# Optimization experiments

Measured on AMD Instinct MI355X. Metric: run time of the kernel, lower is better.

The kernel has to match this reference:

```python
import jax, jax.numpy as jnp
import numpy as np

B, S, D = 2, 2048, 2048
H, G = 32, 8            # n_heads, n_kv_groups
HD = D // H             # head_dim = 64
GS = H // G             # group_size = 4


def _rope(t, cos, sin):
    # t: (B, h, S, HD); cos/sin: (S, HD), start_pos = 0
    half = t.shape[-1] // 2
    rot = jnp.concatenate([-t[..., half:], t[..., :half]], axis=-1)
    return t * cos[None, None] + rot * sin[None, None]


def setup_inputs() -> dict:
    key = jax.random.key(0)
    ks = jax.random.split(key, 7)
    x = jax.random.normal(ks[0], (B, S, D), jnp.float32)
    cos = jax.random.normal(ks[1], (S, HD), jnp.float32)
    sin = jax.random.normal(ks[2], (S, HD), jnp.float32)
    mask = jnp.zeros((S, S), jnp.bool_)
    Wq = jax.random.normal(ks[3], (D, D), jnp.float32) * 0.02
    Wk = jax.random.normal(ks[4], (G * HD, D), jnp.float32) * 0.02
    Wv = jax.random.normal(ks[5], (G * HD, D), jnp.float32) * 0.02
    Wo = jax.random.normal(ks[6], (D, D), jnp.float32) * 0.02
    return {"x": x, "cos": cos, "sin": sin, "mask": mask,
            "Wq": Wq, "Wk": Wk, "Wv": Wv, "Wo": Wo}


def reference(x, cos, sin, mask, Wq, Wk, Wv, Wo):
    b, s, d = x.shape
    # projections (nn.Linear: y = x @ W.T)
    q = (x @ Wq.T).reshape(b, s, H, HD).transpose(0, 2, 1, 3)   # (b,H,s,HD)
    k = (x @ Wk.T).reshape(b, s, G, HD).transpose(0, 2, 1, 3)   # (b,G,s,HD)
    v = (x @ Wv.T).reshape(b, s, G, HD).transpose(0, 2, 1, 3)   # (b,G,s,HD)
    q = _rope(q, cos, sin)
    k = _rope(k, cos, sin)
    # GQA: heads grouped contiguously per kv group (equivalent to repeat_interleave on kv)
    qg = q.reshape(b, G, GS, s, HD)
    scores = jnp.einsum('bgmsd,bgtd->bgmst', qg, k) / jnp.sqrt(jnp.float32(HD))
    # NOTE: original calls non-inplace masked_fill and DISCARDS the result,
    # so the mask has no effect on the output; reproduced faithfully.
    attn = jax.nn.softmax(scores, axis=-1)
    y = jnp.einsum('bgmst,bgtd->bgmsd', attn, v)
    y = y.reshape(b, H, s, HD).transpose(0, 2, 1, 3).reshape(b, s, d)
    return y @ Wo.T
```

## Files before the change

kernel.cpp:

```cpp
#include <hip/hip_runtime.h>
#include <hip/hip_bf16.h>
#include <stdint.h>

#define B_ 2
#define S_ 2048
#define D_ 2048
#define H_ 32
#define G_ 8
#define HD_ 64
#define KVD (G_*HD_)

typedef unsigned short u16;
typedef unsigned int u32;
typedef __attribute__((ext_vector_type(8))) short s8v;
typedef __attribute__((ext_vector_type(4))) float f4v;

static __device__ __forceinline__ float bf2f(u16 u){ return __uint_as_float(((u32)u)<<16); }
static __device__ __forceinline__ u16 f2bf(float f){
  u32 b = __float_as_uint(f);
  return (u16)((b + 0x7FFFu + ((b>>16)&1u)) >> 16);
}
static __device__ __forceinline__ u32 pk2bf(float a, float b){
  float2 f2 = make_float2(a, b);
  __hip_bfloat162 h = __float22bfloat162_rn(f2);
  return *(u32*)&h;
}

struct CvtArgs {
  const float *x, *wq, *wk, *wv, *wo;
  u16 *xb, *wqb, *wkb, *wvb, *wob;
};
__global__ void k_cvt5(CvtArgs a){
  const int E0 = 2097152;
  const int E1 = E0 + 1048576;
  const int E2 = E1 + 262144;
  const int E3 = E2 + 262144;
  const int E4 = E3 + 1048576;
  int u = blockIdx.x*blockDim.x + threadIdx.x;
  int stride = gridDim.x*blockDim.x;
  for (; u < E4; u += stride){
    const float* s; u16* d; int off;
    if      (u < E0){ s = a.x;  d = a.xb;  off = u; }
    else if (u < E1){ s = a.wq; d = a.wqb; off = u - E0; }
    else if (u < E2){ s = a.wk; d = a.wkb; off = u - E1; }
    else if (u < E3){ s = a.wv; d = a.wvb; off = u - E2; }
    else            { s = a.wo; d = a.wob; off = u - E3; }
    float4 f = *(const float4*)(s + (long)off*4);
    uint2 o;
    o.x = (u32)f2bf(f.x) | ((u32)f2bf(f.y)<<16);
    o.y = (u32)f2bf(f.z) | ((u32)f2bf(f.w)<<16);
    *(uint2*)(d + (long)off*4) = o;
  }
}

template<int MODE>
__global__ __launch_bounds__(256) void k_gemm(const u16* __restrict__ A,
    const u16* __restrict__ Bw, const u16* __restrict__ Bw2,
    void* __restrict__ C, void* __restrict__ C2,
    const float* __restrict__ cs, const float* __restrict__ sn,
    int M, int N, int K){
  bool second = (MODE == 2) && (blockIdx.z == 1);
  if (second) Bw = Bw2;
  __shared__ u16 As[128*32];
  __shared__ u16 Bs[128*32];
  const int tid = threadIdx.x;
  const int lane = tid & 63, wid = tid >> 6;
  const int l15 = lane & 15, l4 = lane >> 4;
  const int wr = wid >> 1, wc = wid & 1;
  const long Arow0 = (long)blockIdx.x * 128;
  const long Brow0 = (long)blockIdx.y * 128;
  f4v acc[4][4] = {};
  for (int k0 = 0; k0 < K; k0 += 32){
    if (k0) __syncthreads();
    #pragma unroll
    for (int is = 0; is < 2; ++is){
      int c = (is*4 + wid)*64 + lane;
      int row = c >> 2, slot = c & 3;
      int ko = slot ^ (row & 3);
      const u16* srcA = A + (Arow0 + row)*K + k0 + ko*8;
      const u16* srcB = Bw + (Brow0 + row)*K + k0 + ko*8;
      __builtin_amdgcn_global_load_lds((__attribute__((address_space(1))) void*)(void*)srcA,
          (__attribute__((address_space(3))) void*)(As + (is*4 + wid)*512), 16, 0, 0);
      __builtin_amdgcn_global_load_lds((__attribute__((address_space(1))) void*)(void*)srcB,
          (__attribute__((address_space(3))) void*)(Bs + (is*4 + wid)*512), 16, 0, 0);
    }
    __syncthreads();
    s8v af[4], bf[4];
    #pragma unroll
    for (int m = 0; m < 4; ++m){
      int row = wr*64 + m*16 + l15;
      af[m] = *(const s8v*)((const char*)As + row*64 + ((l4 ^ (row & 3))<<4));
    }
    #pragma unroll
    for (int n = 0; n < 4; ++n){
      int col = wc*64 + n*16 + l15;
      bf[n] = *(const s8v*)((const char*)Bs + col*64 + ((l4 ^ (col & 3))<<4));
    }
    #pragma unroll
    for (int m = 0; m < 4; ++m)
      #pragma unroll
      for (int n = 0; n < 4; ++n)
        acc[m][n] = __builtin_amdgcn_mfma_f32_16x16x32_bf16(af[m], bf[n], acc[m][n], 0, 0, 0);
  }

  if (MODE == 0){
    #pragma unroll
    for (int m = 0; m < 4; ++m)
      #pragma unroll
      for (int n = 0; n < 4; ++n)
        #pragma unroll
        for (int i = 0; i < 4; ++i){
          long r = Arow0 + wr*64 + m*16 + l4*4 + i;
          long c = Brow0 + wc*64 + n*16 + l15;
          ((float*)C)[r*N + c] = acc[m][n][i];
        }
  } else if (MODE == 1 || !second){
    u16* out = (u16*)C;
    #pragma unroll
    for (int m = 0; m < 4; ++m){
      long r0 = Arow0 + wr*64 + m*16 + l4*4;
      #pragma unroll
      for (int i = 0; i < 4; ++i){
        int s = (int)((r0 + i) & (S_-1));
        const float* cb = cs + s*64 + l15;
        const float* sb = sn + s*64 + l15;
        #pragma unroll
        for (int n = 0; n < 2; ++n){
          float c0 = cb[n*16],      s0v = sb[n*16];
          float c1 = cb[n*16 + 32], s1v = sb[n*16 + 32];
          float t0 = acc[m][n][i], t1 = acc[m][n+2][i];
          long cA = Brow0 + wc*64 + n*16 + l15;
          out[(r0+i)*N + cA]      = f2bf(t0*c0 - t1*s0v);
          out[(r0+i)*N + cA + 32] = f2bf(t1*c1 + t0*s1v);
        }
      }
    }
  } else {
    u16* vt = (u16*)C2;
    int g = (int)((Brow0 + wc*64) >> 6);
    #pragma unroll
    for (int m = 0; m < 4; ++m){
      long r0 = Arow0 + wr*64 + m*16 + l4*4;
      int b = (int)(r0 >> 11), s0 = (int)(r0 & (S_-1));
      #pragma unroll
      for (int n = 0; n < 4; ++n){
        int d = n*16 + l15;
        uint2 w;
        w.x = (u32)f2bf(acc[m][n][0]) | ((u32)f2bf(acc[m][n][1])<<16);
        w.y = (u32)f2bf(acc[m][n][2]) | ((u32)f2bf(acc[m][n][3])<<16);
        *(uint2*)(vt + ((long)(b*G_ + g)*64 + d)*S_ + s0) = w;
      }
    }
  }
}

__global__ __launch_bounds__(512) void k_fattn(const u16* __restrict__ q,
    const u16* __restrict__ k, const u16* __restrict__ vt, u16* __restrict__ o){
  __shared__ u16 Ks[3][64*64];
  __shared__ u16 VTs[3][64*64];
  __shared__ u16 Ps[8][32*64];
  const int tid = threadIdx.x, lane = tid & 63, wid = tid >> 6;
  const int l15 = lane & 15, l4 = lane >> 4;
  const int qt = blockIdx.x, h = blockIdx.y, b = blockIdx.z;
  const int g = h >> 2;
  const long qrow0 = (long)b*S_ + qt*256 + wid*32;
  const float C1 = 0.125f * 1.44269504f;
  const float C0 = -8.0f * 1.44269504f;
  const int NT = S_/64;

  s8v aq[2][2];
  #pragma unroll
  for (int mf = 0; mf < 2; ++mf)
    #pragma unroll
    for (int kf = 0; kf < 2; ++kf)
      aq[mf][kf] = *(const s8v*)(q + (qrow0 + mf*16 + l15)*D_ + h*64 + kf*32 + l4*8);

  const int c = wid*64 + lane;
  const int srow = c >> 3, ko = (c & 7) ^ (srow & 7);
  const u16* ksrc0 = k  + ((long)b*S_ + srow)*KVD + g*64 + ko*8;
  const u16* vsrc0 = vt + ((long)(b*G_ + g)*64 + srow)*S_ + ko*8;

  auto stage = [&](int kt, int slot){
    __builtin_amdgcn_global_load_lds(
        (__attribute__((address_space(1))) void*)(void*)(ksrc0 + (long)kt*64*KVD),
        (__attribute__((address_space(3))) void*)(&Ks[slot][wid*512]), 16, 0, 0);
    __builtin_amdgcn_global_load_lds(
        (__attribute__((address_space(1))) void*)(void*)(vsrc0 + kt*64),
        (__attribute__((address_space(3))) void*)(&VTs[slot][wid*512]), 16, 0, 0);
  };

  f4v oacc[2][4] = {};
  float lsum[2] = {0.f, 0.f};

  stage(0, 0);
  stage(1, 1);
  int cur = 0, nxt = 2;
  for (int kt = 0; kt < NT; ++kt){
    asm volatile("s_waitcnt vmcnt(2)" ::: "memory");
    __builtin_amdgcn_s_barrier();
    __builtin_amdgcn_sched_barrier(0);
    stage((kt + 2) & (NT - 1), nxt);
    const u16* KsB = Ks[cur];
    const u16* VsB = VTs[cur];

    s8v bk[4][2];
    #pragma unroll
    for (int nf = 0; nf < 4; ++nf){
      int key = nf*16 + l15;
      #pragma unroll
      for (int kf = 0; kf < 2; ++kf)
        bk[nf][kf] = *(const s8v*)((const char*)KsB + key*128 + (((kf*4 + l4) ^ (key & 7))<<4));
    }
    f4v sacc[2][4] = {};
    __builtin_amdgcn_s_setprio(1);
    #pragma unroll
    for (int mf = 0; mf < 2; ++mf)
      #pragma unroll
      for (int nf = 0; nf < 4; ++nf)
        #pragma unroll
        for (int kf = 0; kf < 2; ++kf)
          sacc[mf][nf] = __builtin_amdgcn_mfma_f32_16x16x32_bf16(bk[nf][kf], aq[mf][kf], sacc[mf][nf], 0, 0, 0);
    __builtin_amdgcn_s_setprio(0);

    #pragma unroll
    for (int mf = 0; mf < 2; ++mf){
      int r = mf*16 + l15;
      char* pbase = (char*)Ps[wid] + r*128 + (l4 & 1)*8;
      float rs = 0.f;
      #pragma unroll
      for (int nf = 0; nf < 4; ++nf){
        float p0 = __builtin_amdgcn_exp2f(fmaf(sacc[mf][nf][0], C1, C0));
        float p1 = __builtin_amdgcn_exp2f(fmaf(sacc[mf][nf][1], C1, C0));
        float p2 = __builtin_amdgcn_exp2f(fmaf(sacc[mf][nf][2], C1, C0));
        float p3 = __builtin_amdgcn_exp2f(fmaf(sacc[mf][nf][3], C1, C0));
        rs += (p0 + p1) + (p2 + p3);
        uint2 w; w.x = pk2bf(p0, p1); w.y = pk2bf(p2, p3);
        int slot = nf*2 + (l4 >> 1);
        *(uint2*)(pbase + ((slot ^ (r & 7))<<4)) = w;
      }
      lsum[mf] += rs;
    }

    s8v ap[2][2];
    #pragma unroll
    for (int mf = 0; mf < 2; ++mf){
      int r = mf*16 + l15;
      #pragma unroll
      for (int kf = 0; kf < 2; ++kf)
        ap[mf][kf] = *(const s8v*)((const char*)Ps[wid] + r*128 + (((kf*4 + l4) ^ (r & 7))<<4));
    }
    __builtin_amdgcn_s_setprio(1);
    #pragma unroll
    for (int nd = 0; nd < 4; ++nd){
      int d = nd*16 + l15;
      #pragma unroll
      for (int kf = 0; kf < 2; ++kf){
        s8v bv = *(const s8v*)((const char*)VsB + d*128 + (((kf*4 + l4) ^ (d & 7))<<4));
        #pragma unroll
        for (int mf = 0; mf < 2; ++mf)
          oacc[mf][nd] = __builtin_amdgcn_mfma_f32_16x16x32_bf16(ap[mf][kf], bv, oacc[mf][nd], 0, 0, 0);
      }
    }
    __builtin_amdgcn_s_setprio(0);
    cur = (cur == 2) ? 0 : cur + 1;
    nxt = (nxt == 2) ? 0 : nxt + 1;
  }

  #pragma unroll
  for (int mf = 0; mf < 2; ++mf){
    lsum[mf] += __shfl_xor(lsum[mf], 16);
    lsum[mf] += __shfl_xor(lsum[mf], 32);
  }
  #pragma unroll
  for (int mf = 0; mf < 2; ++mf){
    float li0 = 1.f / __shfl(lsum[mf], l4*4 + 0);
    float li1 = 1.f / __shfl(lsum[mf], l4*4 + 1);
    float li2 = 1.f / __shfl(lsum[mf], l4*4 + 2);
    float li3 = 1.f / __shfl(lsum[mf], l4*4 + 3);
    #pragma unroll
    for (int nd = 0; nd < 4; ++nd){
      long r = qrow0 + mf*16 + l4*4;
      int cc = h*64 + nd*16 + l15;
      o[(r+0)*D_ + cc] = f2bf(oacc[mf][nd][0]*li0);
      o[(r+1)*D_ + cc] = f2bf(oacc[mf][nd][1]*li1);
      o[(r+2)*D_ + cc] = f2bf(oacc[mf][nd][2]*li2);
      o[(r+3)*D_ + cc] = f2bf(oacc[mf][nd][3]*li3);
    }
  }
}

extern "C" void kernel_launch(void* const* d_in, const int* in_sizes, int n_in,
                              void* d_out, int out_size, void* d_ws, size_t ws_size,
                              hipStream_t stream){
  const float* x    = (const float*)d_in[0];
  const float* cosp = (const float*)d_in[1];
  const float* sinp = (const float*)d_in[2];
  const float* Wq = (const float*)d_in[4];
  const float* Wk = (const float*)d_in[5];
  const float* Wv = (const float*)d_in[6];
  const float* Wo = (const float*)d_in[7];

  char* ws = (char*)d_ws;
  size_t off = 0;
  auto alloc = [&](size_t bytes)->char*{
    char* p = ws + off; off += (bytes + 255) & ~(size_t)255; return p;
  };
  u16* xb  = (u16*)alloc((size_t)8388608*2);
  u16* wqb = (u16*)alloc((size_t)4194304*2);
  u16* wkb = (u16*)alloc((size_t)1048576*2);
  u16* wvb = (u16*)alloc((size_t)1048576*2);
  u16* wob = (u16*)alloc((size_t)4194304*2);
  u16* qb  = (u16*)alloc((size_t)8388608*2);
  u16* kb  = (u16*)alloc((size_t)2097152*2);
  u16* vtb = (u16*)alloc((size_t)2097152*2);
  u16* ab  = (u16*)alloc((size_t)8388608*2);
  if (ws_size < off) return;

  CvtArgs ca{ x, Wq, Wk, Wv, Wo, xb, wqb, wkb, wvb, wob };
  k_cvt5<<<2048,256,0,stream>>>(ca);

  k_gemm<1><<<dim3(32,16,1),256,0,stream>>>(xb, wqb, nullptr, qb, nullptr, cosp, sinp, 4096, 2048, 2048);
  k_gemm<2><<<dim3(32,4,2),256,0,stream>>>(xb, wkb, wvb, kb, vtb, cosp, sinp, 4096, 512, 2048);

  k_fattn<<<dim3(8,32,2),512,0,stream>>>(qb, kb, vtb, ab);

  k_gemm<0><<<dim3(32,16,1),256,0,stream>>>(ab, wob, nullptr, d_out, nullptr, nullptr, nullptr, 4096, 2048, 2048);
}
```

Measured before the change: 248.1 us.

## Switch flash attention to 32x32x16 MFMA and keep P in registers

Rewrites the attention inner loop to use 32x32x16 bf16 MFMA instead of 16x16x32. S is computed transposed (keys × queries), so its output layout maps onto the A-operand layout of the PV MFMA through a single cross-half lane shuffle. This removes the per-wave LDS round trip for the probability tile and its buffer. It also sets launch bounds to two blocks per CU, which adds register pressure and a shuffle cost in exchange for fewer instructions and less LDS traffic.

```diff
diff --git a/kernel.cpp b/kernel.cpp
--- a/kernel.cpp
+++ b/kernel.cpp
@@ -14,6 +14,8 @@
 typedef unsigned int u32;
 typedef __attribute__((ext_vector_type(8))) short s8v;
 typedef __attribute__((ext_vector_type(4))) float f4v;
+typedef __attribute__((ext_vector_type(16))) float f16v;
+typedef __attribute__((ext_vector_type(4))) unsigned int u4v;
 
 static __device__ __forceinline__ float bf2f(u16 u){ return __uint_as_float(((u32)u)<<16); }
 static __device__ __forceinline__ u16 f2bf(float f){
@@ -154,13 +156,12 @@
   }
 }
 
-__global__ __launch_bounds__(512) void k_fattn(const u16* __restrict__ q,
+__global__ __launch_bounds__(512,2) void k_fattn(const u16* __restrict__ q,
     const u16* __restrict__ k, const u16* __restrict__ vt, u16* __restrict__ o){
   __shared__ u16 Ks[3][64*64];
   __shared__ u16 VTs[3][64*64];
-  __shared__ u16 Ps[8][32*64];
   const int tid = threadIdx.x, lane = tid & 63, wid = tid >> 6;
-  const int l15 = lane & 15, l4 = lane >> 4;
+  const int l31 = lane & 31, l32 = lane >> 5;
   const int qt = blockIdx.x, h = blockIdx.y, b = blockIdx.z;
   const int g = h >> 2;
   const long qrow0 = (long)b*S_ + qt*256 + wid*32;
@@ -168,12 +169,10 @@
   const float C0 = -8.0f * 1.44269504f;
   const int NT = S_/64;
 
-  s8v aq[2][2];
+  s8v aq[4];
   #pragma unroll
-  for (int mf = 0; mf < 2; ++mf)
-    #pragma unroll
-    for (int kf = 0; kf < 2; ++kf)
-      aq[mf][kf] = *(const s8v*)(q + (qrow0 + mf*16 + l15)*D_ + h*64 + kf*32 + l4*8);
+  for (int ks = 0; ks < 4; ++ks)
+    aq[ks] = *(const s8v*)(q + (qrow0 + l31)*D_ + h*64 + ks*16 + l32*8);
 
   const int c = wid*64 + lane;
   const int srow = c >> 3, ko = (c & 7) ^ (srow & 7);
@@ -189,8 +188,8 @@
         (__attribute__((address_space(3))) void*)(&VTs[slot][wid*512]), 16, 0, 0);
   };
 
-  f4v oacc[2][4] = {};
-  float lsum[2] = {0.f, 0.f};
+  f16v oacc[2] = {};
+  float lsum = 0.f;
 
   stage(0, 0);
   stage(1, 1);
@@ -203,90 +202,93 @@
     const u16* KsB = Ks[cur];
     const u16* VsB = VTs[cur];
 
-    s8v bk[4][2];
-    #pragma unroll
-    for (int nf = 0; nf < 4; ++nf){
-      int key = nf*16 + l15;
-      #pragma unroll
-      for (int kf = 0; kf < 2; ++kf)
-        bk[nf][kf] = *(const s8v*)((const char*)KsB + key*128 + (((kf*4 + l4) ^ (key & 7))<<4));
-    }
-    f4v sacc[2][4] = {};
+    s8v bkk[2][4];
+    #pragma unroll
+    for (int nf = 0; nf < 2; ++nf){
+      int key = nf*32 + l31;
+      #pragma unroll
+      for (int ks = 0; ks < 4; ++ks)
+        bkk[nf][ks] = *(const s8v*)((const char*)KsB + key*128 + (((ks*2 + l32) ^ (key & 7))<<4));
+    }
+    f16v sacc[2] = {};
     __builtin_amdgcn_s_setprio(1);
     #pragma unroll
-    for (int mf = 0; mf < 2; ++mf)
-      #pragma unroll
-      for (int nf = 0; nf < 4; ++nf)
-        #pragma unroll
-        for (int kf = 0; kf < 2; ++kf)
-          sacc[mf][nf] = __builtin_amdgcn_mfma_f32_16x16x32_bf16(bk[nf][kf], aq[mf][kf], sacc[mf][nf], 0, 0, 0);
+    for (int ks = 0; ks < 4; ++ks)
+      #pragma unroll
+      for (int nf = 0; nf < 2; ++nf)
+        sacc[nf] = __builtin_amdgcn_mfma_f32_32x32x16_bf16(bkk[nf][ks], aq[ks], sacc[nf], 0, 0, 0);
     __builtin_amdgcn_s_setprio(0);
 
-    #pragma unroll
-    for (int mf = 0; mf < 2; ++mf){
-      int r = mf*16 + l15;
-      char* pbase = (char*)Ps[wid] + r*128 + (l4 & 1)*8;
-      float rs = 0.f;
-      #pragma unroll
-      for (int nf = 0; nf < 4; ++nf){
-        float p0 = __builtin_amdgcn_exp2f(fmaf(sacc[mf][nf][0], C1, C0));
-        float p1 = __builtin_amdgcn_exp2f(fmaf(sacc[mf][nf][1], C1, C0));
-        float p2 = __builtin_amdgcn_exp2f(fmaf(sacc[mf][nf][2], C1, C0));
-        float p3 = __builtin_amdgcn_exp2f(fmaf(sacc[mf][nf][3], C1, C0));
+    u32 w[2][8];
+    float rs = 0.f;
+    #pragma unroll
+    for (int nf = 0; nf < 2; ++nf){
+      #pragma unroll
+      for (int t = 0; t < 4; ++t){
+        float p0 = __builtin_amdgcn_exp2f(fmaf(sacc[nf][4*t+0], C1, C0));
+        float p1 = __builtin_amdgcn_exp2f(fmaf(sacc[nf][4*t+1], C1, C0));
+        float p2 = __builtin_amdgcn_exp2f(fmaf(sacc[nf][4*t+2], C1, C0));
+        float p3 = __builtin_amdgcn_exp2f(fmaf(sacc[nf][4*t+3], C1, C0));
         rs += (p0 + p1) + (p2 + p3);
-        uint2 w; w.x = pk2bf(p0, p1); w.y = pk2bf(p2, p3);
-        int slot = nf*2 + (l4 >> 1);
-        *(uint2*)(pbase + ((slot ^ (r & 7))<<4)) = w;
+        w[nf][2*t]   = pk2bf(p0, p1);
+        w[nf][2*t+1] = pk2bf(p2, p3);
       }
-      lsum[mf] += rs;
-    }
-
-    s8v ap[2][2];
-    #pragma unroll
-    for (int mf = 0; mf < 2; ++mf){
-      int r = mf*16 + l15;
-      #pragma unroll
-      for (int kf = 0; kf < 2; ++kf)
-        ap[mf][kf] = *(const s8v*)((const char*)Ps[wid] + r*128 + (((kf*4 + l4) ^ (r & 7))<<4));
+    }
+    lsum += rs;
+
+    s8v pa[4];
+    #pragma unroll
+    for (int s = 0; s < 4; ++s){
+      int nf = s >> 1, base = (s & 1)*4;
+      u32 w0 = w[nf][base+0], w1 = w[nf][base+1];
+      u32 w2 = w[nf][base+2], w3 = w[nf][base+3];
+      u32 sel02 = l32 ? w0 : w2;
+      u32 sel13 = l32 ? w1 : w3;
+      u32 t02 = (u32)__shfl_xor((int)sel02, 32);
+      u32 t13 = (u32)__shfl_xor((int)sel13, 32);
+      u4v uv;
+      uv.x = l32 ? t02 : w0;
+      uv.y = l32 ? t13 : w1;
+      uv.z = l32 ? w2 : t02;
+      uv.w = l32 ? w3 : t13;
+      pa[s] = *(s8v*)&uv;
+    }
+
+    s8v bv[2][4];
+    #pragma unroll
+    for (int nd = 0; nd < 2; ++nd){
+      int d = nd*32 + l31;
+      #pragma unroll
+      for (int s = 0; s < 4; ++s)
+        bv[nd][s] = *(const s8v*)((const char*)VsB + d*128 + (((s*2 + l32) ^ (d & 7))<<4));
     }
     __builtin_amdgcn_s_setprio(1);
     #pragma unroll
-    for (int nd = 0; nd < 4; ++nd){
-      int d = nd*16 + l15;
-      #pragma unroll
-      for (int kf = 0; kf < 2; ++kf){
-        s8v bv = *(const s8v*)((const char*)VsB + d*128 + (((kf*4 + l4) ^ (d & 7))<<4));
-        #pragma unroll
-        for (int mf = 0; mf < 2; ++mf)
-          oacc[mf][nd] = __builtin_amdgcn_mfma_f32_16x16x32_bf16(ap[mf][kf], bv, oacc[mf][nd], 0, 0, 0);
-      }
-    }
+    for (int s = 0; s < 4; ++s)
+      #pragma unroll
+      for (int nd = 0; nd < 2; ++nd)
+        oacc[nd] = __builtin_amdgcn_mfma_f32_32x32x16_bf16(pa[s], bv[nd][s], oacc[nd], 0, 0, 0);
     __builtin_amdgcn_s_setprio(0);
+
     cur = (cur == 2) ? 0 : cur + 1;
     nxt = (nxt == 2) ? 0 : nxt + 1;
   }
 
+  lsum += __shfl_xor(lsum, 32);
+  float linv = 1.f / lsum;
+  float li[16];
   #pragma unroll
-  for (int mf = 0; mf < 2; ++mf){
-    lsum[mf] += __shfl_xor(lsum[mf], 16);
-    lsum[mf] += __shfl_xor(lsum[mf], 32);
+  for (int reg = 0; reg < 16; ++reg){
+    int qp = (reg & 3) + 8*(reg >> 2) + 4*l32;
+    li[reg] = __shfl(linv, qp);
   }
   #pragma unroll
-  for (int mf = 0; mf < 2; ++mf){
-    float li0 = 1.f / __shfl(lsum[mf], l4*4 + 0);
-    float li1 = 1.f / __shfl(lsum[mf], l4*4 + 1);
-    float li2 = 1.f / __shfl(lsum[mf], l4*4 + 2);
-    float li3 = 1.f / __shfl(lsum[mf], l4*4 + 3);
-    #pragma unroll
-    for (int nd = 0; nd < 4; ++nd){
-      long r = qrow0 + mf*16 + l4*4;
-      int cc = h*64 + nd*16 + l15;
-      o[(r+0)*D_ + cc] = f2bf(oacc[mf][nd][0]*li0);
-      o[(r+1)*D_ + cc] = f2bf(oacc[mf][nd][1]*li1);
-      o[(r+2)*D_ + cc] = f2bf(oacc[mf][nd][2]*li2);
-      o[(r+3)*D_ + cc] = f2bf(oacc[mf][nd][3]*li3);
-    }
-  }
+  for (int nd = 0; nd < 2; ++nd)
+    #pragma unroll
+    for (int reg = 0; reg < 16; ++reg){
+      int qp = (reg & 3) + 8*(reg >> 2) + 4*l32;
+      o[(qrow0 + qp)*D_ + h*64 + nd*32 + l31] = f2bf(oacc[nd][reg] * li[reg]);
+    }
 }
 
 extern "C" void kernel_launch(void* const* d_in, const int* in_sizes, int n_in,
```

Measured after the change: 257.0 us. +3.6%, slower.

## Fuse Q/K/V projections into one GEMM and double-buffer attention K/V

Applied to the files above, without the earlier changes.

Concatenates Wq, Wk and Wv into a single bf16 weight buffer and computes all three projections in one GEMM launch. The epilogue routes columns to Q or K (with RoPE) or to transposed V. Separately, the attention kernel's K/V staging changes from a three-slot ring with partial vmcnt waits to a two-slot double buffer with a full block barrier. This reduces launch count and LDS usage, but lowers prefetch depth and may expose more load latency in attention.

```diff
diff --git a/kernel.cpp b/kernel.cpp
--- a/kernel.cpp
+++ b/kernel.cpp
@@ -28,7 +28,7 @@
 
 struct CvtArgs {
   const float *x, *wq, *wk, *wv, *wo;
-  u16 *xb, *wqb, *wkb, *wvb, *wob;
+  u16 *xb, *wqkvb, *wob;
 };
 __global__ void k_cvt5(CvtArgs a){
   const int E0 = 2097152;
@@ -40,11 +40,11 @@
   int stride = gridDim.x*blockDim.x;
   for (; u < E4; u += stride){
     const float* s; u16* d; int off;
-    if      (u < E0){ s = a.x;  d = a.xb;  off = u; }
-    else if (u < E1){ s = a.wq; d = a.wqb; off = u - E0; }
-    else if (u < E2){ s = a.wk; d = a.wkb; off = u - E1; }
-    else if (u < E3){ s = a.wv; d = a.wvb; off = u - E2; }
-    else            { s = a.wo; d = a.wob; off = u - E3; }
+    if      (u < E0){ s = a.x;  d = a.xb;               off = u; }
+    else if (u < E1){ s = a.wq; d = a.wqkvb;            off = u - E0; }
+    else if (u < E2){ s = a.wk; d = a.wqkvb + 4194304;  off = u - E1; }
+    else if (u < E3){ s = a.wv; d = a.wqkvb + 5242880;  off = u - E2; }
+    else            { s = a.wo; d = a.wob;              off = u - E3; }
     float4 f = *(const float4*)(s + (long)off*4);
     uint2 o;
     o.x = (u32)f2bf(f.x) | ((u32)f2bf(f.y)<<16);
@@ -55,12 +55,10 @@
 
 template<int MODE>
 __global__ __launch_bounds__(256) void k_gemm(const u16* __restrict__ A,
-    const u16* __restrict__ Bw, const u16* __restrict__ Bw2,
-    void* __restrict__ C, void* __restrict__ C2,
+    const u16* __restrict__ Bw,
+    void* __restrict__ C, void* __restrict__ C2, void* __restrict__ C3,
     const float* __restrict__ cs, const float* __restrict__ sn,
-    int M, int N, int K){
-  bool second = (MODE == 2) && (blockIdx.z == 1);
-  if (second) Bw = Bw2;
+    int N_unused, int K){
   __shared__ u16 As[128*32];
   __shared__ u16 Bs[128*32];
   const int tid = threadIdx.x;
@@ -112,43 +110,48 @@
         for (int i = 0; i < 4; ++i){
           long r = Arow0 + wr*64 + m*16 + l4*4 + i;
           long c = Brow0 + wc*64 + n*16 + l15;
-          ((float*)C)[r*N + c] = acc[m][n][i];
+          ((float*)C)[r*2048 + c] = acc[m][n][i];
         }
-  } else if (MODE == 1 || !second){
-    u16* out = (u16*)C;
-    #pragma unroll
-    for (int m = 0; m < 4; ++m){
-      long r0 = Arow0 + wr*64 + m*16 + l4*4;
-      #pragma unroll
-      for (int i = 0; i < 4; ++i){
-        int s = (int)((r0 + i) & (S_-1));
-        const float* cb = cs + s*64 + l15;
-        const float* sb = sn + s*64 + l15;
-        #pragma unroll
-        for (int n = 0; n < 2; ++n){
-          float c0 = cb[n*16],      s0v = sb[n*16];
-          float c1 = cb[n*16 + 32], s1v = sb[n*16 + 32];
-          float t0 = acc[m][n][i], t1 = acc[m][n+2][i];
-          long cA = Brow0 + wc*64 + n*16 + l15;
-          out[(r0+i)*N + cA]      = f2bf(t0*c0 - t1*s0v);
-          out[(r0+i)*N + cA + 32] = f2bf(t1*c1 + t0*s1v);
+  } else {
+    const long col0 = Brow0 + wc*64;
+    if (col0 < 2560){
+      u16* out; long cbase; int stride;
+      if (col0 < 2048){ out = (u16*)C;  cbase = col0;        stride = 2048; }
+      else            { out = (u16*)C2; cbase = col0 - 2048; stride = 512;  }
+      #pragma unroll
+      for (int m = 0; m < 4; ++m){
+        long r0 = Arow0 + wr*64 + m*16 + l4*4;
+        #pragma unroll
+        for (int i = 0; i < 4; ++i){
+          int s = (int)((r0 + i) & (S_-1));
+          const float* cb = cs + s*64 + l15;
+          const float* sb = sn + s*64 + l15;
+          #pragma unroll
+          for (int n = 0; n < 2; ++n){
+            float c0 = cb[n*16],      s0v = sb[n*16];
+            float c1 = cb[n*16 + 32], s1v = sb[n*16 + 32];
+            float t0 = acc[m][n][i], t1 = acc[m][n+2][i];
+            long cA = cbase + n*16 + l15;
+            out[(r0+i)*stride + cA]      = f2bf(t0*c0 - t1*s0v);
+            out[(r0+i)*stride + cA + 32] = f2bf(t1*c1 + t0*s1v);
+          }
         }
       }
-    }
-  } else {
-    u16* vt = (u16*)C2;
-    int g = (int)((Brow0 + wc*64) >> 6);
-    #pragma unroll
-    for (int m = 0; m < 4; ++m){
-      long r0 = Arow0 + wr*64 + m*16 + l4*4;
-      int b = (int)(r0 >> 11), s0 = (int)(r0 & (S_-1));
-      #pragma unroll
-      for (int n = 0; n < 4; ++n){
-        int d = n*16 + l15;
-        uint2 w;
-        w.x = (u32)f2bf(acc[m][n][0]) | ((u32)f2bf(acc[m][n][1])<<16);
-        w.y = (u32)f2bf(acc[m][n][2]) | ((u32)f2bf(acc[m][n][3])<<16);
-        *(uint2*)(vt + ((long)(b*G_ + g)*64 + d)*S_ + s0) = w;
+    } else {
+      u16* vt = (u16*)C3;
+      int g = (int)((col0 - 2560) >> 6);
+      #pragma unroll
+      for (int m = 0; m < 4; ++m){
+        long r0 = Arow0 + wr*64 + m*16 + l4*4;
+        int b = (int)(r0 >> 11), s0 = (int)(r0 & (S_-1));
+        #pragma unroll
+        for (int n = 0; n < 4; ++n){
+          int d = n*16 + l15;
+          uint2 w;
+          w.x = (u32)f2bf(acc[m][n][0]) | ((u32)f2bf(acc[m][n][1])<<16);
+          w.y = (u32)f2bf(acc[m][n][2]) | ((u32)f2bf(acc[m][n][3])<<16);
+          *(uint2*)(vt + ((long)(b*G_ + g)*64 + d)*S_ + s0) = w;
+        }
       }
     }
   }
@@ -156,8 +159,8 @@
 
 __global__ __launch_bounds__(512) void k_fattn(const u16* __restrict__ q,
     const u16* __restrict__ k, const u16* __restrict__ vt, u16* __restrict__ o){
-  __shared__ u16 Ks[3][64*64];
-  __shared__ u16 VTs[3][64*64];
+  __shared__ u16 Ks[2][64*64];
+  __shared__ u16 VTs[2][64*64];
   __shared__ u16 Ps[8][32*64];
   const int tid = threadIdx.x, lane = tid & 63, wid = tid >> 6;
   const int l15 = lane & 15, l4 = lane >> 4;
@@ -166,7 +169,6 @@
   const long qrow0 = (long)b*S_ + qt*256 + wid*32;
   const float C1 = 0.125f * 1.44269504f;
   const float C0 = -8.0f * 1.44269504f;
-  const int NT = S_/64;
 
   s8v aq[2][2];
   #pragma unroll
@@ -180,28 +182,25 @@
   const u16* ksrc0 = k  + ((long)b*S_ + srow)*KVD + g*64 + ko*8;
   const u16* vsrc0 = vt + ((long)(b*G_ + g)*64 + srow)*S_ + ko*8;
 
-  auto stage = [&](int kt, int slot){
+  auto stage = [&](int kt){
+    int bsel = kt & 1;
     __builtin_amdgcn_global_load_lds(
         (__attribute__((address_space(1))) void*)(void*)(ksrc0 + (long)kt*64*KVD),
-        (__attribute__((address_space(3))) void*)(&Ks[slot][wid*512]), 16, 0, 0);
+        (__attribute__((address_space(3))) void*)(&Ks[bsel][wid*512]), 16, 0, 0);
     __builtin_amdgcn_global_load_lds(
         (__attribute__((address_space(1))) void*)(void*)(vsrc0 + kt*64),
-        (__attribute__((address_space(3))) void*)(&VTs[slot][wid*512]), 16, 0, 0);
+        (__attribute__((address_space(3))) void*)(&VTs[bsel][wid*512]), 16, 0, 0);
   };
 
   f4v oacc[2][4] = {};
   float lsum[2] = {0.f, 0.f};
 
-  stage(0, 0);
-  stage(1, 1);
-  int cur = 0, nxt = 2;
-  for (int kt = 0; kt < NT; ++kt){
-    asm volatile("s_waitcnt vmcnt(2)" ::: "memory");
-    __builtin_amdgcn_s_barrier();
-    __builtin_amdgcn_sched_barrier(0);
-    stage((kt + 2) & (NT - 1), nxt);
-    const u16* KsB = Ks[cur];
-    const u16* VsB = VTs[cur];
+  stage(0);
+  for (int kt = 0; kt < S_/64; ++kt){
+    __syncthreads();
+    if (kt + 1 < S_/64) stage(kt + 1);
+    const u16* KsB = Ks[kt & 1];
+    const u16* VsB = VTs[kt & 1];
 
     s8v bk[4][2];
     #pragma unroll
@@ -262,8 +261,6 @@
       }
     }
     __builtin_amdgcn_s_setprio(0);
-    cur = (cur == 2) ? 0 : cur + 1;
-    nxt = (nxt == 2) ? 0 : nxt + 1;
   }
 
   #pragma unroll
@@ -305,24 +302,21 @@
   auto alloc = [&](size_t bytes)->char*{
     char* p = ws + off; off += (bytes + 255) & ~(size_t)255; return p;
   };
-  u16* xb  = (u16*)alloc((size_t)8388608*2);
-  u16* wqb = (u16*)alloc((size_t)4194304*2);
-  u16* wkb = (u16*)alloc((size_t)1048576*2);
-  u16* wvb = (u16*)alloc((size_t)1048576*2);
-  u16* wob = (u16*)alloc((size_t)4194304*2);
-  u16* qb  = (u16*)alloc((size_t)8388608*2);
-  u16* kb  = (u16*)alloc((size_t)2097152*2);
-  u16* vtb = (u16*)alloc((size_t)2097152*2);
-  u16* ab  = (u16*)alloc((size_t)8388608*2);
+  u16* xb    = (u16*)alloc((size_t)8388608*2);
+  u16* wqkvb = (u16*)alloc((size_t)6291456*2);
+  u16* wob   = (u16*)alloc((size_t)4194304*2);
+  u16* qb    = (u16*)alloc((size_t)8388608*2);
+  u16* kb    = (u16*)alloc((size_t)2097152*2);
+  u16* vtb   = (u16*)alloc((size_t)2097152*2);
+  u16* ab    = (u16*)alloc((size_t)8388608*2);
   if (ws_size < off) return;
 
-  CvtArgs ca{ x, Wq, Wk, Wv, Wo, xb, wqb, wkb, wvb, wob };
+  CvtArgs ca{ x, Wq, Wk, Wv, Wo, xb, wqkvb, wob };
   k_cvt5<<<2048,256,0,stream>>>(ca);
 
-  k_gemm<1><<<dim3(32,16,1),256,0,stream>>>(xb, wqb, nullptr, qb, nullptr, cosp, sinp, 4096, 2048, 2048);
-  k_gemm<2><<<dim3(32,4,2),256,0,stream>>>(xb, wkb, wvb, kb, vtb, cosp, sinp, 4096, 512, 2048);
+  k_gemm<3><<<dim3(32,24,1),256,0,stream>>>(xb, wqkvb, qb, kb, vtb, cosp, sinp, 3072, 2048);
 
   k_fattn<<<dim3(8,32,2),512,0,stream>>>(qb, kb, vtb, ab);
 
-  k_gemm<0><<<dim3(32,16,1),256,0,stream>>>(ab, wob, nullptr, d_out, nullptr, nullptr, nullptr, 4096, 2048, 2048);
-}
+  k_gemm<0><<<dim3(32,16,1),256,0,stream>>>(ab, wob, d_out, nullptr, nullptr, nullptr, nullptr, 2048, 2048);
+}
```

After: 242.1 us. -2.4%, faster.
